# Performance work log

Hardware: AMD Instinct MI355X
Metric: run time of the kernel (lower is better)

Reference implementation:

```python
import jax, jax.numpy as jnp
import numpy as np

B, T, F2, F1 = 64, 300, 2944, 1472
RED, H, K, LN = 256, 32, 15, 7          # reduced_size, hidden_size, att_frams, layer_num
CA_RED = 320
N_CROP = T - 2 * (K - 1)                # 272 frames after the two k=15 convs
PYR = [2 ** j for j in range(1, LN)]    # [2,4,8,16,32,64]


def _pool_matrix(N, sizes):
    """Stacked AdaptiveAvgPool1d matrices: rows average torch-style bins."""
    mats = []
    for m in sizes:
        P = np.zeros((m, N), np.float32)
        for i in range(m):
            s = (i * N) // m
            e = -((-(i + 1) * N) // m)  # ceil((i+1)*N/m)
            P[i, s:e] = 1.0 / (e - s)
        mats.append(P)
    return jnp.asarray(np.concatenate(mats, 0))  # [sum(sizes), N]


def setup_inputs() -> dict:
    key = jax.random.key(0)
    ks = jax.random.split(key, 24)
    g = lambda k, sh, s=0.05: (jax.random.normal(k, sh) * s).astype(jnp.float32)
    inp = {
        "input": jax.random.normal(ks[0], (B, T, F2), jnp.float32),
        "input_length": jnp.full((B,), T, jnp.int64),
        "mean_var": g(ks[1], (F1,), 1.0),
        "std_var": jax.random.uniform(ks[2], (F1,), jnp.float32, 0.5, 1.5),
        "mean_mean": g(ks[3], (F1,), 1.0),
        "std_mean": jax.random.uniform(ks[4], (F1,), jnp.float32, 0.5, 1.5),
        # ChannelAttention params
        "ca_fc1_w": g(ks[5], (CA_RED, F2)), "ca_fc1_b": g(ks[6], (CA_RED,)),
        "ca_fc2_w": g(ks[7], (F2, CA_RED)), "ca_fc2_b": g(ks[8], (F2,)),
        # ANN (n_ANNlayers=1 -> only fc0 used)
        "ann_w": g(ks[9], (RED, F1)), "ann_b": g(ks[10], (RED,)),
        # GRU (torch gate order r,z,n)
        "gru_w_ih": g(ks[11], (3 * H, RED)), "gru_w_hh": g(ks[12], (3 * H, H)),
        "gru_b_ih": g(ks[13], (3 * H,)), "gru_b_hh": g(ks[14], (3 * H,)),
        # frame-quality head
        "q_w": g(ks[15], (1, H)), "q_b": g(ks[16], (1,)),
        # temporal attention convs
        "att_w1": g(ks[17], (1, H, K)), "att_b1": g(ks[18], (1,)),
        "att_w2": g(ks[19], (1, 1, K)), "att_b2": g(ks[20], (1,)),
        "qreg2_w": g(ks[21], (1, 2 ** LN - 1)), "qreg2_b": g(ks[22], (1,)),
    }
    return inp


def _gru(x, w_ih, w_hh, b_ih, b_hh):
    xg = jnp.einsum("btf,gf->btg", x, w_ih) + b_ih  # [B,T,3H]

    def step(h, xt):
        hg = h @ w_hh.T + b_hh
        xr, xz, xn = jnp.split(xt, 3, -1)
        hr, hz, hn = jnp.split(hg, 3, -1)
        r = jax.nn.sigmoid(xr + hr)
        z = jax.nn.sigmoid(xz + hz)
        n = jnp.tanh(xn + r * hn)
        h = (1.0 - z) * n + z * h
        return h, h

    h0 = jnp.zeros((x.shape[0], H), x.dtype)
    _, hs = jax.lax.scan(step, h0, jnp.swapaxes(xg, 0, 1))
    return jnp.swapaxes(hs, 0, 1)  # [B,T,H]


def reference(input, input_length, mean_var, std_var, mean_mean, std_mean,
              ca_fc1_w, ca_fc1_b, ca_fc2_w, ca_fc2_b, ann_w, ann_b,
              gru_w_ih, gru_w_hh, gru_b_ih, gru_b_hh, q_w, q_b,
              att_w1, att_b1, att_w2, att_b2, qreg2_w, qreg2_b):
    # --- ChannelAttention: normalize var/mean halves, sigmoid gate, fuse to 1472-d
    x_var = (input[..., :F1] - mean_var) / std_var
    x_mean = (input[..., F1:] - mean_mean) / std_mean
    xn = jnp.concatenate([x_var, x_mean], -1)                      # [B,T,2944]
    w = jax.nn.sigmoid(jnp.maximum(xn @ ca_fc1_w.T + ca_fc1_b, 0.0) @ ca_fc2_w.T + ca_fc2_b)
    feat = w[..., :F1] * x_var + w[..., F1:] * x_mean              # [B,T,1472]

    # --- ANN (single layer) + GRU
    feat = feat @ ann_w.T + ann_b                                  # [B,T,256]
    outs = _gru(feat, gru_w_ih, gru_w_hh, gru_b_ih, gru_b_hh)      # [B,T,32]

    # --- temporal attention: Conv1d(H,1,15) -> ReLU -> Conv1d(1,1,15) -> tanh
    xc = jnp.swapaxes(outs, 1, 2)                                  # [B,H,T]
    dn = ("NCH", "OIH", "NCH")
    a = jax.lax.conv_general_dilated(xc, att_w1, (1,), "VALID", dimension_numbers=dn) + att_b1[None, :, None]
    a = jnp.maximum(a, 0.0)
    a = jax.lax.conv_general_dilated(a, att_w2, (1,), "VALID", dimension_numbers=dn) + att_b2[None, :, None]
    att = jnp.tanh(a[:, 0, :])                                     # [B,N_CROP]

    q_fet = att[..., None] * outs[:, K - 1: T - (K - 1), :]        # [B,N_CROP,H]

    # --- pyramid pooling: row0 = plain mean, rest = attention-weighted means
    P = _pool_matrix(N_CROP, PYR)                                  # [126, N_CROP]
    row0 = q_fet.mean(1, keepdims=True)                            # [B,1,H]
    num = jnp.einsum("mn,bnh->bmh", P, q_fet)                      # [B,126,H]
    den = jnp.einsum("mn,bn->bm", P, att)[..., None]               # [B,126,1]
    q_pool = jnp.concatenate([row0, num / den], 1)                 # [B,127,H]

    q_each = (q_pool @ q_w.T + q_b)[..., 0]                        # [B,127]
    score = q_each @ qreg2_w.T + qreg2_b                           # [B,1]
    return score
```

## Files before the change

### kernel.cpp

```cpp
#include <hip/hip_runtime.h>


typedef unsigned short u16t;
typedef unsigned int   u32t;
typedef float  f32x4 __attribute__((ext_vector_type(4)));
typedef u32t   u32x4 __attribute__((ext_vector_type(4)));
typedef __bf16 bf16x8 __attribute__((ext_vector_type(8)));

__device__ __forceinline__ f32x4 mfma_b(u32x4 a, u32x4 b, f32x4 c){
  return __builtin_amdgcn_mfma_f32_16x16x32_bf16(
      __builtin_bit_cast(bf16x8, a), __builtin_bit_cast(bf16x8, b), c, 0, 0, 0);
}

#define GLDS16(SRC, DST)                                                    \
  __builtin_amdgcn_global_load_lds(                                         \
      (const __attribute__((address_space(1))) void*)(SRC),                 \
      (__attribute__((address_space(3))) void*)(DST), 16, 0, 0)

__device__ __forceinline__ void split3(float x, u16t& h, u16t& m, u16t& l){
  u32t u = __float_as_uint(x);
  h = (u16t)(u >> 16);
  float d1 = x - __uint_as_float(u & 0xFFFF0000u);
  u32t u1 = __float_as_uint(d1);
  m = (u16t)(u1 >> 16);
  float d2 = d1 - __uint_as_float(u1 & 0xFFFF0000u);
  l = (u16t)(__float_as_uint(d2) >> 16);
}

__device__ __forceinline__ u32t resid(u32t u){
  float d = __uint_as_float(u) - __uint_as_float(u & 0xFFFF0000u);
  return __float_as_uint(d);
}

__device__ __forceinline__ void split8_3(u32x4 a, u32x4 b,
                                         u32x4& H, u32x4& M, u32x4& L){
  u32t r1[8], r2[8];
#pragma unroll
  for (int j = 0; j < 4; j++){ r1[j] = resid(a[j]); r1[4 + j] = resid(b[j]); }
#pragma unroll
  for (int j = 0; j < 8; j++){ r2[j] = resid(r1[j]); }
  H[0] = __builtin_amdgcn_perm(a[1], a[0], 0x07060302u);
  H[1] = __builtin_amdgcn_perm(a[3], a[2], 0x07060302u);
  H[2] = __builtin_amdgcn_perm(b[1], b[0], 0x07060302u);
  H[3] = __builtin_amdgcn_perm(b[3], b[2], 0x07060302u);
  M[0] = __builtin_amdgcn_perm(r1[1], r1[0], 0x07060302u);
  M[1] = __builtin_amdgcn_perm(r1[3], r1[2], 0x07060302u);
  M[2] = __builtin_amdgcn_perm(r1[5], r1[4], 0x07060302u);
  M[3] = __builtin_amdgcn_perm(r1[7], r1[6], 0x07060302u);
  L[0] = __builtin_amdgcn_perm(r2[1], r2[0], 0x07060302u);
  L[1] = __builtin_amdgcn_perm(r2[3], r2[2], 0x07060302u);
  L[2] = __builtin_amdgcn_perm(r2[5], r2[4], 0x07060302u);
  L[3] = __builtin_amdgcn_perm(r2[7], r2[6], 0x07060302u);
}

__device__ __forceinline__ void mfma6(const u32x4& AH, const u32x4& AM, const u32x4& AL,
                                      const u32x4& BH, const u32x4& BM, const u32x4& BL,
                                      f32x4& acc){
  acc = mfma_b(AL, BH, acc);
  acc = mfma_b(AM, BM, acc);
  acc = mfma_b(AH, BL, acc);
  acc = mfma_b(AM, BH, acc);
  acc = mfma_b(AH, BM, acc);
  acc = mfma_b(AH, BH, acc);
}

__global__ __launch_bounds__(256) void prep_params_kernel(
    const float* __restrict__ mv, const float* __restrict__ sv,
    const float* __restrict__ mm, const float* __restrict__ sm,
    double* __restrict__ mu, double* __restrict__ rinv){
  int f = blockIdx.x * 256 + threadIdx.x;
  if (f < 2944){
    if (f < 1472){ mu[f] = (double)mv[f]; rinv[f] = 1.0 / (double)sv[f]; }
    else         { mu[f] = (double)mm[f - 1472]; rinv[f] = 1.0 / (double)sm[f - 1472]; }
  }
}

__global__ __launch_bounds__(256) void split3_w1_kernel(
    const float* __restrict__ w, const double* __restrict__ rinv,
    u16t* __restrict__ wh, u16t* __restrict__ wm, u16t* __restrict__ wl){
  int id = blockIdx.x * 256 + threadIdx.x;
  if (id < 320 * 2944){
    float v = (float)((double)w[id] * rinv[id % 2944]);
    split3(v, wh[id], wm[id], wl[id]);
  }
}

__global__ __launch_bounds__(256) void split3_plain_kernel(
    const float* __restrict__ w, u16t* __restrict__ wh, u16t* __restrict__ wm,
    u16t* __restrict__ wl, int n){
  int id = blockIdx.x * 256 + threadIdx.x;
  if (id < n) split3(w[id], wh[id], wm[id], wl[id]);
}

__global__ __launch_bounds__(64) void b1p_kernel(
    const float* __restrict__ w1, const float* __restrict__ b1,
    const double* __restrict__ mu, const double* __restrict__ rinv,
    float* __restrict__ b1p){
  int n = blockIdx.x, lane = threadIdx.x;
  double s = 0.0;
  for (int k = lane; k < 2944; k += 64)
    s += (double)w1[n * 2944 + k] * rinv[k] * mu[k];
#pragma unroll
  for (int o = 32; o > 0; o >>= 1) s += __shfl_xor(s, o);
  if (lane == 0) b1p[n] = (float)((double)b1[n] - s);
}

__global__ __launch_bounds__(256) void make_wc_kernel(
    const float* __restrict__ wih, const float* __restrict__ annw,
    const float* __restrict__ annb, const float* __restrict__ bih,
    u16t* __restrict__ wch, u16t* __restrict__ wcm, u16t* __restrict__ wcl,
    float* __restrict__ bc){
  int id = blockIdx.x * 256 + threadIdx.x;
  if (id < 96 * 1472){
    int g = id / 1472, k = id - g * 1472;
    double s = 0.0;
    for (int r = 0; r < 256; r++)
      s += (double)wih[g * 256 + r] * (double)annw[r * 1472 + k];
    split3((float)s, wch[id], wcm[id], wcl[id]);
  } else if (id < 96 * 1472 + 96){
    int g = id - 96 * 1472;
    double s = (double)bih[g];
    for (int r = 0; r < 256; r++)
      s += (double)wih[g * 256 + r] * (double)annb[r];
    bc[g] = (float)s;
  }
}

__global__ __launch_bounds__(256) void gemm1_kernel(
    const float* __restrict__ x,
    const u16t* __restrict__ w1h, const u16t* __restrict__ w1m,
    const u16t* __restrict__ w1l, const float* __restrict__ b1p,
    u16t* __restrict__ h1h, u16t* __restrict__ h1m, u16t* __restrict__ h1l){
  __shared__ float lA[64 * 32];
  __shared__ u16t lBh[160 * 32], lBm[160 * 32], lBl[160 * 32];
  const int tid = threadIdx.x, wave = tid >> 6, lane = tid & 63;
  const int wm = wave >> 1, wn = wave & 1;
  const int bid = blockIdx.x;
  const int xcd = bid & 7, j = bid >> 3;
  const int mg = xcd + ((j >> 1) << 3);
  if (mg >= 300) return;
  const int m0 = mg * 64, n0 = (j & 1) * 160;
  const int ar = lane >> 3, as = lane & 7;
  const int br = lane >> 2, bs = lane & 3;
  f32x4 acc[2][5] = {};
  for (int k0 = 0; k0 < 2944; k0 += 32){
    __syncthreads();
#pragma unroll
    for (int i = wave; i < 8; i += 4){
      int row = i * 8 + ar;
      GLDS16(x + (size_t)(m0 + row) * 2944 + k0 + ((as ^ (row & 7)) << 2), lA + (i << 8));
    }
    for (int i = wave; i < 10; i += 4){
      int row = i * 16 + br;
      size_t src = (size_t)(n0 + row) * 2944 + k0 + ((bs ^ ((row >> 1) & 3)) << 3);
      GLDS16(w1h + src, lBh + (i << 9));
      GLDS16(w1m + src, lBm + (i << 9));
      GLDS16(w1l + src, lBl + (i << 9));
    }
    __syncthreads();
    const int g = lane >> 4, r15 = lane & 15;
    u32x4 AH[2], AM[2], AL[2];
#pragma unroll
    for (int fm = 0; fm < 2; fm++){
      int row = wm * 32 + fm * 16 + r15;
      const char* base = (const char*)lA + (row << 7);
      u32x4 a0 = *(const u32x4*)(base + ((((g << 1) + 0) ^ (row & 7)) << 4));
      u32x4 a1 = *(const u32x4*)(base + ((((g << 1) + 1) ^ (row & 7)) << 4));
      split8_3(a0, a1, AH[fm], AM[fm], AL[fm]);
    }
#pragma unroll
    for (int fn = 0; fn < 5; fn++){
      int row = wn * 80 + fn * 16 + r15;
      int off = (row << 6) + ((g ^ ((row >> 1) & 3)) << 4);
      u32x4 BH = *(const u32x4*)((const char*)lBh + off);
      u32x4 BM = *(const u32x4*)((const char*)lBm + off);
      u32x4 BL = *(const u32x4*)((const char*)lBl + off);
#pragma unroll
      for (int fm = 0; fm < 2; fm++)
        mfma6(AH[fm], AM[fm], AL[fm], BH, BM, BL, acc[fm][fn]);
    }
  }
#pragma unroll
  for (int fn = 0; fn < 5; fn++){
    int col = n0 + wn * 80 + fn * 16 + (lane & 15);
    float bias = b1p[col];
#pragma unroll
    for (int fm = 0; fm < 2; fm++){
      int mb = m0 + wm * 32 + fm * 16 + ((lane >> 4) << 2);
#pragma unroll
      for (int r = 0; r < 4; r++){
        float v = fmaxf(acc[fm][fn][r] + bias, 0.f);
        size_t o = (size_t)(mb + r) * 320 + col;
        split3(v, h1h[o], h1m[o], h1l[o]);
      }
    }
  }
}

__global__ __launch_bounds__(256) void gemm2_kernel(
    const u16t* __restrict__ h1h, const u16t* __restrict__ h1m,
    const u16t* __restrict__ h1l,
    const u16t* __restrict__ w2h, const u16t* __restrict__ w2m,
    const u16t* __restrict__ w2l, const float* __restrict__ b2,
    const float* __restrict__ x, const double* __restrict__ mu,
    const double* __restrict__ rinv,
    u16t* __restrict__ feath, u16t* __restrict__ featm, u16t* __restrict__ featl){
  __shared__ u16t lAh[96 * 32], lAm[96 * 32], lAl[96 * 32];
  __shared__ u16t lBh[128 * 32], lBm[128 * 32], lBl[128 * 32];
  const int tid = threadIdx.x, wave = tid >> 6, lane = tid & 63;
  const int wm = wave >> 1, wn = wave & 1;
  const int bid = blockIdx.x;
  const int xcd = bid & 7, j = bid >> 3;
  const int q = j / 23, f0i = j - q * 23;
  const int mg = xcd + (q << 3);
  if (mg >= 200) return;
  const int m0 = mg * 96, f0 = f0i * 64;
  const int br = lane >> 2, bs = lane & 3;
  f32x4 acc[3][4] = {};
  for (int k0 = 0; k0 < 320; k0 += 32){
    __syncthreads();
    for (int i = wave; i < 6; i += 4){
      int row = i * 16 + br;
      int cs = (bs ^ ((row >> 1) & 3)) << 3;
      size_t sa = (size_t)(m0 + row) * 320 + k0 + cs;
      GLDS16(h1h + sa, lAh + (i << 9));
      GLDS16(h1m + sa, lAm + (i << 9));
      GLDS16(h1l + sa, lAl + (i << 9));
    }
    for (int i = wave; i < 8; i += 4){
      int row = i * 16 + br;
      int cs = (bs ^ ((row >> 1) & 3)) << 3;
      int w2row = (((row >> 4) & 1) * 1472) + f0 + ((row >> 5) << 4) + (row & 15);
      size_t sb = (size_t)w2row * 320 + k0 + cs;
      GLDS16(w2h + sb, lBh + (i << 9));
      GLDS16(w2m + sb, lBm + (i << 9));
      GLDS16(w2l + sb, lBl + (i << 9));
    }
    __syncthreads();
    const int g = lane >> 4, r15 = lane & 15;
    u32x4 AH[3], AM[3], AL[3];
#pragma unroll
    for (int fm = 0; fm < 3; fm++){
      int row = wm * 48 + fm * 16 + r15;
      int off = (row << 6) + ((g ^ ((row >> 1) & 3)) << 4);
      AH[fm] = *(const u32x4*)((const char*)lAh + off);
      AM[fm] = *(const u32x4*)((const char*)lAm + off);
      AL[fm] = *(const u32x4*)((const char*)lAl + off);
    }
#pragma unroll
    for (int fn = 0; fn < 4; fn++){
      int row = wn * 64 + fn * 16 + r15;
      int off = (row << 6) + ((g ^ ((row >> 1) & 3)) << 4);
      u32x4 BH = *(const u32x4*)((const char*)lBh + off);
      u32x4 BM = *(const u32x4*)((const char*)lBm + off);
      u32x4 BL = *(const u32x4*)((const char*)lBl + off);
#pragma unroll
      for (int fm = 0; fm < 3; fm++)
        mfma6(AH[fm], AM[fm], AL[fm], BH, BM, BL, acc[fm][fn]);
    }
  }
#pragma unroll
  for (int cg = 0; cg < 2; cg++){
    int f = f0 + wn * 32 + cg * 16 + (lane & 15);
    float blo = b2[f], bhi = b2[1472 + f];
    double muv = mu[f], riv = rinv[f];
    double mum = mu[1472 + f], rim = rinv[1472 + f];
#pragma unroll
    for (int fm = 0; fm < 3; fm++){
      int mb = m0 + wm * 48 + fm * 16 + ((lane >> 4) << 2);
#pragma unroll
      for (int r = 0; r < 4; r++){
        int m = mb + r;
        float zl = acc[fm][2 * cg][r] + blo;
        float zh = acc[fm][2 * cg + 1][r] + bhi;
        float wl = 1.f / (1.f + expf(-zl));
        float wh = 1.f / (1.f + expf(-zh));
        float xv = (float)(((double)x[(size_t)m * 2944 + f] - muv) * riv);
        float xm = (float)(((double)x[(size_t)m * 2944 + 1472 + f] - mum) * rim);
        float fv = wl * xv + wh * xm;
        size_t o = (size_t)m * 1472 + f;
        split3(fv, feath[o], featm[o], featl[o]);
      }
    }
  }
}

__global__ __launch_bounds__(256) void gemm3_kernel(
    const u16t* __restrict__ feath, const u16t* __restrict__ featm,
    const u16t* __restrict__ featl,
    const u16t* __restrict__ wch, const u16t* __restrict__ wcm,
    const u16t* __restrict__ wcl, const float* __restrict__ bc,
    float* __restrict__ xg){
  __shared__ u16t lAh[64 * 32], lAm[64 * 32], lAl[64 * 32];
  __shared__ u16t lBh[96 * 32], lBm[96 * 32], lBl[96 * 32];
  const int tid = threadIdx.x, wave = tid >> 6, lane = tid & 63;
  const int wm = wave >> 1, wn = wave & 1;
  const int m0 = blockIdx.x * 64;
  const int br = lane >> 2, bs = lane & 3;
  f32x4 acc[2][3] = {};
  for (int k0 = 0; k0 < 1472; k0 += 32){
    __syncthreads();
#pragma unroll
    for (int i = wave; i < 4; i += 4){
      int row = i * 16 + br;
      int cs = (bs ^ ((row >> 1) & 3)) << 3;
      size_t sa = (size_t)(m0 + row) * 1472 + k0 + cs;
      GLDS16(feath + sa, lAh + (i << 9));
      GLDS16(featm + sa, lAm + (i << 9));
      GLDS16(featl + sa, lAl + (i << 9));
    }
    for (int i = wave; i < 6; i += 4){
      int row = i * 16 + br;
      int cs = (bs ^ ((row >> 1) & 3)) << 3;
      size_t sb = (size_t)row * 1472 + k0 + cs;
      GLDS16(wch + sb, lBh + (i << 9));
      GLDS16(wcm + sb, lBm + (i << 9));
      GLDS16(wcl + sb, lBl + (i << 9));
    }
    __syncthreads();
    const int g = lane >> 4, r15 = lane & 15;
    u32x4 AH[2], AM[2], AL[2];
#pragma unroll
    for (int fm = 0; fm < 2; fm++){
      int row = wm * 32 + fm * 16 + r15;
      int off = (row << 6) + ((g ^ ((row >> 1) & 3)) << 4);
      AH[fm] = *(const u32x4*)((const char*)lAh + off);
      AM[fm] = *(const u32x4*)((const char*)lAm + off);
      AL[fm] = *(const u32x4*)((const char*)lAl + off);
    }
#pragma unroll
    for (int fn = 0; fn < 3; fn++){
      int row = wn * 48 + fn * 16 + r15;
      int off = (row << 6) + ((g ^ ((row >> 1) & 3)) << 4);
      u32x4 BH = *(const u32x4*)((const char*)lBh + off);
      u32x4 BM = *(const u32x4*)((const char*)lBm + off);
      u32x4 BL = *(const u32x4*)((const char*)lBl + off);
#pragma unroll
      for (int fm = 0; fm < 2; fm++)
        mfma6(AH[fm], AM[fm], AL[fm], BH, BM, BL, acc[fm][fn]);
    }
  }
#pragma unroll
  for (int fn = 0; fn < 3; fn++){
    int col = wn * 48 + fn * 16 + (lane & 15);
    float bias = bc[col];
#pragma unroll
    for (int fm = 0; fm < 2; fm++){
      int mb = m0 + wm * 32 + fm * 16 + ((lane >> 4) << 2);
#pragma unroll
      for (int r = 0; r < 4; r++)
        xg[(size_t)(mb + r) * 96 + col] = acc[fm][fn][r] + bias;
    }
  }
}

__global__ __launch_bounds__(128) void gru_kernel(
    const float* __restrict__ xg, const float* __restrict__ whh,
    const float* __restrict__ bhh, float* __restrict__ outs){
  const int b = blockIdx.x, tid = threadIdx.x;
  __shared__ float hs[32];
  __shared__ double hg[96];
  double wr[32];
  double bias = 0.0;
  if (tid < 96){
#pragma unroll
    for (int j = 0; j < 32; j++) wr[j] = (double)whh[tid * 32 + j];
    bias = (double)bhh[tid];
  }
  if (tid < 32) hs[tid] = 0.f;
  __syncthreads();
  const float* xb = xg + (size_t)b * 300 * 96;
  float* ob = outs + (size_t)b * 300 * 32;
  for (int t = 0; t < 300; t++){
    if (tid < 96){
      double s0 = 0.0, s1 = 0.0;
#pragma unroll
      for (int j = 0; j < 16; j++){
        s0 += wr[j] * (double)hs[j];
        s1 += wr[16 + j] * (double)hs[16 + j];
      }
      hg[tid] = bias + s0 + s1;
    }
    __syncthreads();
    if (tid < 32){
      float xr  = xb[t * 96 + tid];
      float xz  = xb[t * 96 + 32 + tid];
      float xnv = xb[t * 96 + 64 + tid];
      float r = 1.f / (1.f + expf(-(float)((double)xr + hg[tid])));
      float z = 1.f / (1.f + expf(-(float)((double)xz + hg[32 + tid])));
      float n = tanhf((float)((double)xnv + (double)r * hg[64 + tid]));
      float h = (1.f - z) * n + z * hs[tid];
      hs[tid] = h;
      ob[t * 32 + tid] = h;
    }
    __syncthreads();
  }
}

__global__ __launch_bounds__(64) void attn_final_kernel(
    const float* __restrict__ outs, const float* __restrict__ w1,
    const float* __restrict__ b1, const float* __restrict__ w2,
    const float* __restrict__ b2, const float* __restrict__ qw,
    const float* __restrict__ qb, const float* __restrict__ rw,
    const float* __restrict__ rb, float* __restrict__ out){
  const int b = blockIdx.x, lane = threadIdx.x;
  __shared__ float a1[286];
  __shared__ double attv[272];
  __shared__ double sd[272];
  __shared__ float w1s[480];
  __shared__ float qws[32];
  const float* ob = outs + (size_t)b * 300 * 32;
  for (int i = lane; i < 480; i += 64) w1s[i] = w1[i];
  if (lane < 32) qws[lane] = qw[lane];
  __syncthreads();
  const double bb1 = (double)b1[0];
  for (int t = lane; t < 286; t += 64){
    double s = bb1;
    for (int k = 0; k < 15; k++){
      const float* row = ob + (t + k) * 32;
#pragma unroll
      for (int c = 0; c < 32; c++) s += (double)row[c] * (double)w1s[c * 15 + k];
    }
    a1[t] = fmaxf((float)s, 0.f);
  }
  __syncthreads();
  const double bb2 = (double)b2[0];
  for (int t = lane; t < 272; t += 64){
    double s = bb2;
#pragma unroll
    for (int k = 0; k < 15; k++) s += (double)a1[t + k] * (double)w2[k];
    double a = tanh(s);
    attv[t] = a;
    const float* row = ob + (t + 14) * 32;
    double d = 0.0;
#pragma unroll
    for (int c = 0; c < 32; c++) d += (double)row[c] * (double)qws[c];
    sd[t] = a * d;
  }
  __syncthreads();
  const double qb0 = (double)qb[0];
  double part = 0.0;
  double msum = 0.0;
  for (int t = lane; t < 272; t += 64) msum += sd[t];
  part += (double)rw[0] * (msum / 272.0);
  if (lane == 0) part += (double)rw[0] * qb0 + (double)rb[0];
  for (int j = lane; j < 126; j += 64){
    int mcur = 2, i = j;
    while (i >= mcur){ i -= mcur; mcur <<= 1; }
    int s = (i * 272) / mcur;
    int e = ((i + 1) * 272 + mcur - 1) / mcur;
    double S = 0.0, A = 0.0;
    for (int n = s; n < e; n++){ S += sd[n]; A += attv[n]; }
    part += (double)rw[1 + j] * (S / A + qb0);
  }
#pragma unroll
  for (int o = 32; o > 0; o >>= 1) part += __shfl_xor(part, o);
  if (lane == 0) out[b] = (float)part;
}

extern "C" void kernel_launch(void* const* d_in, const int* in_sizes, int n_in,
                              void* d_out, int out_size, void* d_ws, size_t ws_size,
                              hipStream_t stream){
  const float* input     = (const float*)d_in[0];
  const float* mean_var  = (const float*)d_in[2];
  const float* std_var   = (const float*)d_in[3];
  const float* mean_mean = (const float*)d_in[4];
  const float* std_mean  = (const float*)d_in[5];
  const float* ca1w = (const float*)d_in[6];
  const float* ca1b = (const float*)d_in[7];
  const float* ca2w = (const float*)d_in[8];
  const float* ca2b = (const float*)d_in[9];
  const float* annw = (const float*)d_in[10];
  const float* annb = (const float*)d_in[11];
  const float* wih  = (const float*)d_in[12];
  const float* whh  = (const float*)d_in[13];
  const float* bih  = (const float*)d_in[14];
  const float* bhh  = (const float*)d_in[15];
  const float* qw   = (const float*)d_in[16];
  const float* qb   = (const float*)d_in[17];
  const float* aw1  = (const float*)d_in[18];
  const float* ab1  = (const float*)d_in[19];
  const float* aw2  = (const float*)d_in[20];
  const float* ab2  = (const float*)d_in[21];
  const float* rw   = (const float*)d_in[22];
  const float* rb   = (const float*)d_in[23];
  float* out = (float*)d_out;

  char* ws = (char*)d_ws;
  size_t off = 0;
  auto alloc = [&](size_t bytes){
    size_t o = off; off += (bytes + 255) & ~(size_t)255; return o;
  };
  const size_t H1 = (size_t)19200 * 320, FT = (size_t)19200 * 1472;
  u16t* h1h = (u16t*)(ws + alloc(H1 * 2));
  u16t* h1m = (u16t*)(ws + alloc(H1 * 2));
  u16t* h1l = (u16t*)(ws + alloc(H1 * 2));
  u16t* feath = (u16t*)(ws + alloc(FT * 2));
  u16t* featm = (u16t*)(ws + alloc(FT * 2));
  u16t* featl = (u16t*)(ws + alloc(FT * 2));
  float* xg    = (float*)(ws + alloc((size_t)19200 * 96 * 4));
  float* outsb = (float*)(ws + alloc((size_t)19200 * 32 * 4));
  u16t* w1h = (u16t*)(ws + alloc((size_t)320 * 2944 * 2));
  u16t* w1m = (u16t*)(ws + alloc((size_t)320 * 2944 * 2));
  u16t* w1l = (u16t*)(ws + alloc((size_t)320 * 2944 * 2));
  u16t* w2h = (u16t*)(ws + alloc((size_t)2944 * 320 * 2));
  u16t* w2m = (u16t*)(ws + alloc((size_t)2944 * 320 * 2));
  u16t* w2l = (u16t*)(ws + alloc((size_t)2944 * 320 * 2));
  u16t* wch = (u16t*)(ws + alloc((size_t)96 * 1472 * 2));
  u16t* wcm = (u16t*)(ws + alloc((size_t)96 * 1472 * 2));
  u16t* wcl = (u16t*)(ws + alloc((size_t)96 * 1472 * 2));
  double* mu   = (double*)(ws + alloc(2944 * 8));
  double* rinv = (double*)(ws + alloc(2944 * 8));
  float* b1p   = (float*)(ws + alloc(320 * 4));
  float* bc    = (float*)(ws + alloc(96 * 4));
  (void)ws_size; (void)in_sizes; (void)n_in; (void)out_size;

  prep_params_kernel<<<12, 256, 0, stream>>>(mean_var, std_var, mean_mean, std_mean, mu, rinv);
  split3_w1_kernel<<<3680, 256, 0, stream>>>(ca1w, rinv, w1h, w1m, w1l);
  split3_plain_kernel<<<3680, 256, 0, stream>>>(ca2w, w2h, w2m, w2l, 2944 * 320);
  b1p_kernel<<<320, 64, 0, stream>>>(ca1w, ca1b, mu, rinv, b1p);
  make_wc_kernel<<<553, 256, 0, stream>>>(wih, annw, annb, bih, wch, wcm, wcl, bc);
  gemm1_kernel<<<608, 256, 0, stream>>>(input, w1h, w1m, w1l, b1p, h1h, h1m, h1l);
  gemm2_kernel<<<4600, 256, 0, stream>>>(h1h, h1m, h1l, w2h, w2m, w2l, ca2b,
                                         input, mu, rinv, feath, featm, featl);
  gemm3_kernel<<<300, 256, 0, stream>>>(feath, featm, featl, wch, wcm, wcl, bc, xg);
  gru_kernel<<<64, 128, 0, stream>>>(xg, whh, bhh, outsb);
  attn_final_kernel<<<64, 64, 0, stream>>>(outsb, aw1, ab1, aw2, ab2, qw, qb, rw, rb, out);
}
```

Baseline: 926.6 us.

## Fuse channel-attention gating GEMM with GRU input projection via LDS-resident features

Merges gemm2 and gemm3 into one kernel. Each block owns 32 rows and loops over all 23 feature tiles, writing the gated feature tile (split into three bf16 parts) into swizzled LDS. It then immediately multiplies that tile by the combined GRU input weights, which are re-laid out by make_wc_kernel so they can be read directly from global memory. This removes the large three-part feature round-trip through HBM and one kernel launch. The cost is a much smaller M tile, which lowers MFMA reuse per B load, and re-streaming all w2 tiles once per 32-row block, which raises L2 traffic.

```diff
diff --git a/kernel.cpp b/kernel.cpp
--- a/kernel.cpp
+++ b/kernel.cpp
@@ -108,7 +108,7 @@
 __global__ __launch_bounds__(256) void make_wc_kernel(
     const float* __restrict__ wih, const float* __restrict__ annw,
     const float* __restrict__ annb, const float* __restrict__ bih,
-    u16t* __restrict__ wch, u16t* __restrict__ wcm, u16t* __restrict__ wcl,
+    u16t* __restrict__ wcfh, u16t* __restrict__ wcfm, u16t* __restrict__ wcfl,
     float* __restrict__ bc){
   int id = blockIdx.x * 256 + threadIdx.x;
   if (id < 96 * 1472){
@@ -116,7 +116,9 @@
     double s = 0.0;
     for (int r = 0; r < 256; r++)
       s += (double)wih[g * 256 + r] * (double)annw[r * 1472 + k];
-    split3((float)s, wch[id], wcm[id], wcl[id]);
+    size_t o = ((size_t)(k >> 3) * 96 + g) * 8 + (k & 7);
+    u16t hh, mm2, ll; split3((float)s, hh, mm2, ll);
+    wcfh[o] = hh; wcfm[o] = mm2; wcfl[o] = ll;
   } else if (id < 96 * 1472 + 96){
     int g = id - 96 * 1472;
     double s = (double)bih[g];
@@ -197,160 +199,117 @@
   }
 }
 
-__global__ __launch_bounds__(256) void gemm2_kernel(
+__global__ __launch_bounds__(256) void gemm23_kernel(
     const u16t* __restrict__ h1h, const u16t* __restrict__ h1m,
     const u16t* __restrict__ h1l,
     const u16t* __restrict__ w2h, const u16t* __restrict__ w2m,
     const u16t* __restrict__ w2l, const float* __restrict__ b2,
     const float* __restrict__ x, const double* __restrict__ mu,
     const double* __restrict__ rinv,
-    u16t* __restrict__ feath, u16t* __restrict__ featm, u16t* __restrict__ featl){
-  __shared__ u16t lAh[96 * 32], lAm[96 * 32], lAl[96 * 32];
+    const u16t* __restrict__ wcfh, const u16t* __restrict__ wcfm,
+    const u16t* __restrict__ wcfl, const float* __restrict__ bc,
+    float* __restrict__ xg){
+  __shared__ u16t lAh[32 * 32], lAm[32 * 32], lAl[32 * 32];
   __shared__ u16t lBh[128 * 32], lBm[128 * 32], lBl[128 * 32];
+  __shared__ u16t fSh[32 * 64], fSm[32 * 64], fSl[32 * 64];
   const int tid = threadIdx.x, wave = tid >> 6, lane = tid & 63;
   const int wm = wave >> 1, wn = wave & 1;
   const int bid = blockIdx.x;
-  const int xcd = bid & 7, j = bid >> 3;
-  const int q = j / 23, f0i = j - q * 23;
-  const int mg = xcd + (q << 3);
-  if (mg >= 200) return;
-  const int m0 = mg * 96, f0 = f0i * 64;
+  const int mg = (bid & 7) * 75 + (bid >> 3);
+  const int m0 = mg * 32;
   const int br = lane >> 2, bs = lane & 3;
-  f32x4 acc[3][4] = {};
-  for (int k0 = 0; k0 < 320; k0 += 32){
-    __syncthreads();
-    for (int i = wave; i < 6; i += 4){
-      int row = i * 16 + br;
-      int cs = (bs ^ ((row >> 1) & 3)) << 3;
-      size_t sa = (size_t)(m0 + row) * 320 + k0 + cs;
-      GLDS16(h1h + sa, lAh + (i << 9));
-      GLDS16(h1m + sa, lAm + (i << 9));
-      GLDS16(h1l + sa, lAl + (i << 9));
-    }
-    for (int i = wave; i < 8; i += 4){
-      int row = i * 16 + br;
-      int cs = (bs ^ ((row >> 1) & 3)) << 3;
-      int w2row = (((row >> 4) & 1) * 1472) + f0 + ((row >> 5) << 4) + (row & 15);
-      size_t sb = (size_t)w2row * 320 + k0 + cs;
-      GLDS16(w2h + sb, lBh + (i << 9));
-      GLDS16(w2m + sb, lBm + (i << 9));
-      GLDS16(w2l + sb, lBl + (i << 9));
-    }
-    __syncthreads();
-    const int g = lane >> 4, r15 = lane & 15;
-    u32x4 AH[3], AM[3], AL[3];
-#pragma unroll
-    for (int fm = 0; fm < 3; fm++){
-      int row = wm * 48 + fm * 16 + r15;
-      int off = (row << 6) + ((g ^ ((row >> 1) & 3)) << 4);
-      AH[fm] = *(const u32x4*)((const char*)lAh + off);
-      AM[fm] = *(const u32x4*)((const char*)lAm + off);
-      AL[fm] = *(const u32x4*)((const char*)lAl + off);
-    }
-#pragma unroll
-    for (int fn = 0; fn < 4; fn++){
-      int row = wn * 64 + fn * 16 + r15;
-      int off = (row << 6) + ((g ^ ((row >> 1) & 3)) << 4);
-      u32x4 BH = *(const u32x4*)((const char*)lBh + off);
-      u32x4 BM = *(const u32x4*)((const char*)lBm + off);
-      u32x4 BL = *(const u32x4*)((const char*)lBl + off);
-#pragma unroll
-      for (int fm = 0; fm < 3; fm++)
-        mfma6(AH[fm], AM[fm], AL[fm], BH, BM, BL, acc[fm][fn]);
-    }
-  }
-#pragma unroll
-  for (int cg = 0; cg < 2; cg++){
-    int f = f0 + wn * 32 + cg * 16 + (lane & 15);
-    float blo = b2[f], bhi = b2[1472 + f];
-    double muv = mu[f], riv = rinv[f];
-    double mum = mu[1472 + f], rim = rinv[1472 + f];
-#pragma unroll
-    for (int fm = 0; fm < 3; fm++){
-      int mb = m0 + wm * 48 + fm * 16 + ((lane >> 4) << 2);
+  const int g = lane >> 4, r15 = lane & 15;
+  f32x4 acc2[3] = {};
+  for (int f0i = 0; f0i < 23; ++f0i){
+    const int f0 = f0i * 64;
+    f32x4 acc[4] = {};
+    for (int k0 = 0; k0 < 320; k0 += 32){
+      __syncthreads();
+      for (int i = wave; i < 2; i += 4){
+        int row = i * 16 + br;
+        int cs = (bs ^ ((row >> 1) & 3)) << 3;
+        size_t sa = (size_t)(m0 + row) * 320 + k0 + cs;
+        GLDS16(h1h + sa, lAh + (i << 9));
+        GLDS16(h1m + sa, lAm + (i << 9));
+        GLDS16(h1l + sa, lAl + (i << 9));
+      }
+      for (int i = wave; i < 8; i += 4){
+        int row = i * 16 + br;
+        int cs = (bs ^ ((row >> 1) & 3)) << 3;
+        int w2row = (((row >> 4) & 1) * 1472) + f0 + ((row >> 5) << 4) + (row & 15);
+        size_t sb = (size_t)w2row * 320 + k0 + cs;
+        GLDS16(w2h + sb, lBh + (i << 9));
+        GLDS16(w2m + sb, lBm + (i << 9));
+        GLDS16(w2l + sb, lBl + (i << 9));
+      }
+      __syncthreads();
+      int arow = wm * 16 + r15;
+      int aoff = (arow << 6) + ((g ^ ((arow >> 1) & 3)) << 4);
+      u32x4 AH = *(const u32x4*)((const char*)lAh + aoff);
+      u32x4 AM = *(const u32x4*)((const char*)lAm + aoff);
+      u32x4 AL = *(const u32x4*)((const char*)lAl + aoff);
+#pragma unroll
+      for (int fn = 0; fn < 4; fn++){
+        int row = wn * 64 + fn * 16 + r15;
+        int off = (row << 6) + ((g ^ ((row >> 1) & 3)) << 4);
+        u32x4 BH = *(const u32x4*)((const char*)lBh + off);
+        u32x4 BM = *(const u32x4*)((const char*)lBm + off);
+        u32x4 BL = *(const u32x4*)((const char*)lBl + off);
+        mfma6(AH, AM, AL, BH, BM, BL, acc[fn]);
+      }
+    }
+#pragma unroll
+    for (int cg = 0; cg < 2; cg++){
+      int f = f0 + wn * 32 + cg * 16 + r15;
+      float blo = b2[f], bhi = b2[1472 + f];
+      double muv = mu[f], riv = rinv[f];
+      double mum = mu[1472 + f], rim = rinv[1472 + f];
+      int c = wn * 32 + cg * 16 + r15;
+      int mbl = wm * 16 + (g << 2);
 #pragma unroll
       for (int r = 0; r < 4; r++){
-        int m = mb + r;
-        float zl = acc[fm][2 * cg][r] + blo;
-        float zh = acc[fm][2 * cg + 1][r] + bhi;
+        int m = m0 + mbl + r;
+        float zl = acc[2 * cg][r] + blo;
+        float zh = acc[2 * cg + 1][r] + bhi;
         float wl = 1.f / (1.f + expf(-zl));
         float wh = 1.f / (1.f + expf(-zh));
         float xv = (float)(((double)x[(size_t)m * 2944 + f] - muv) * riv);
         float xm = (float)(((double)x[(size_t)m * 2944 + 1472 + f] - mum) * rim);
         float fv = wl * xv + wh * xm;
-        size_t o = (size_t)m * 1472 + f;
-        split3(fv, feath[o], featm[o], featl[o]);
-      }
-    }
-  }
-}
-
-__global__ __launch_bounds__(256) void gemm3_kernel(
-    const u16t* __restrict__ feath, const u16t* __restrict__ featm,
-    const u16t* __restrict__ featl,
-    const u16t* __restrict__ wch, const u16t* __restrict__ wcm,
-    const u16t* __restrict__ wcl, const float* __restrict__ bc,
-    float* __restrict__ xg){
-  __shared__ u16t lAh[64 * 32], lAm[64 * 32], lAl[64 * 32];
-  __shared__ u16t lBh[96 * 32], lBm[96 * 32], lBl[96 * 32];
-  const int tid = threadIdx.x, wave = tid >> 6, lane = tid & 63;
-  const int wm = wave >> 1, wn = wave & 1;
-  const int m0 = blockIdx.x * 64;
-  const int br = lane >> 2, bs = lane & 3;
-  f32x4 acc[2][3] = {};
-  for (int k0 = 0; k0 < 1472; k0 += 32){
+        int lm = mbl + r;
+        int idx = (lm << 6) + (((c >> 3) ^ (lm & 7)) << 3) + (c & 7);
+        u16t hh, mm2, ll; split3(fv, hh, mm2, ll);
+        fSh[idx] = hh; fSm[idx] = mm2; fSl[idx] = ll;
+      }
+    }
     __syncthreads();
 #pragma unroll
-    for (int i = wave; i < 4; i += 4){
-      int row = i * 16 + br;
-      int cs = (bs ^ ((row >> 1) & 3)) << 3;
-      size_t sa = (size_t)(m0 + row) * 1472 + k0 + cs;
-      GLDS16(feath + sa, lAh + (i << 9));
-      GLDS16(featm + sa, lAm + (i << 9));
-      GLDS16(featl + sa, lAl + (i << 9));
-    }
-    for (int i = wave; i < 6; i += 4){
-      int row = i * 16 + br;
-      int cs = (bs ^ ((row >> 1) & 3)) << 3;
-      size_t sb = (size_t)row * 1472 + k0 + cs;
-      GLDS16(wch + sb, lBh + (i << 9));
-      GLDS16(wcm + sb, lBm + (i << 9));
-      GLDS16(wcl + sb, lBl + (i << 9));
-    }
-    __syncthreads();
-    const int g = lane >> 4, r15 = lane & 15;
-    u32x4 AH[2], AM[2], AL[2];
-#pragma unroll
-    for (int fm = 0; fm < 2; fm++){
-      int row = wm * 32 + fm * 16 + r15;
-      int off = (row << 6) + ((g ^ ((row >> 1) & 3)) << 4);
-      AH[fm] = *(const u32x4*)((const char*)lAh + off);
-      AM[fm] = *(const u32x4*)((const char*)lAm + off);
-      AL[fm] = *(const u32x4*)((const char*)lAl + off);
-    }
-#pragma unroll
-    for (int fn = 0; fn < 3; fn++){
-      int row = wn * 48 + fn * 16 + r15;
-      int off = (row << 6) + ((g ^ ((row >> 1) & 3)) << 4);
-      u32x4 BH = *(const u32x4*)((const char*)lBh + off);
-      u32x4 BM = *(const u32x4*)((const char*)lBm + off);
-      u32x4 BL = *(const u32x4*)((const char*)lBl + off);
-#pragma unroll
-      for (int fm = 0; fm < 2; fm++)
-        mfma6(AH[fm], AM[fm], AL[fm], BH, BM, BL, acc[fm][fn]);
+    for (int ks = 0; ks < 2; ks++){
+      int arow = wm * 16 + r15;
+      int slot = (ks * 4 + g) ^ (arow & 7);
+      int aoff = (arow << 7) + (slot << 4);
+      u32x4 AH = *(const u32x4*)((const char*)fSh + aoff);
+      u32x4 AM = *(const u32x4*)((const char*)fSm + aoff);
+      u32x4 AL = *(const u32x4*)((const char*)fSl + aoff);
+#pragma unroll
+      for (int fn = 0; fn < 3; fn++){
+        int grow = wn * 48 + fn * 16 + r15;
+        size_t woff = ((size_t)(f0i * 8 + ks * 4 + g) * 96 + grow) * 8;
+        u32x4 BH = *(const u32x4*)(wcfh + woff);
+        u32x4 BM = *(const u32x4*)(wcfm + woff);
+        u32x4 BL = *(const u32x4*)(wcfl + woff);
+        mfma6(AH, AM, AL, BH, BM, BL, acc2[fn]);
+      }
     }
   }
 #pragma unroll
   for (int fn = 0; fn < 3; fn++){
-    int col = wn * 48 + fn * 16 + (lane & 15);
+    int col = wn * 48 + fn * 16 + r15;
     float bias = bc[col];
-#pragma unroll
-    for (int fm = 0; fm < 2; fm++){
-      int mb = m0 + wm * 32 + fm * 16 + ((lane >> 4) << 2);
-#pragma unroll
-      for (int r = 0; r < 4; r++)
-        xg[(size_t)(mb + r) * 96 + col] = acc[fm][fn][r] + bias;
-    }
+    int mb = m0 + wm * 16 + (g << 2);
+#pragma unroll
+    for (int r = 0; r < 4; r++)
+      xg[(size_t)(mb + r) * 96 + col] = acc2[fn][r] + bias;
   }
 }
 
@@ -491,13 +450,10 @@
   auto alloc = [&](size_t bytes){
     size_t o = off; off += (bytes + 255) & ~(size_t)255; return o;
   };
-  const size_t H1 = (size_t)19200 * 320, FT = (size_t)19200 * 1472;
+  const size_t H1 = (size_t)19200 * 320;
   u16t* h1h = (u16t*)(ws + alloc(H1 * 2));
   u16t* h1m = (u16t*)(ws + alloc(H1 * 2));
   u16t* h1l = (u16t*)(ws + alloc(H1 * 2));
-  u16t* feath = (u16t*)(ws + alloc(FT * 2));
-  u16t* featm = (u16t*)(ws + alloc(FT * 2));
-  u16t* featl = (u16t*)(ws + alloc(FT * 2));
   float* xg    = (float*)(ws + alloc((size_t)19200 * 96 * 4));
   float* outsb = (float*)(ws + alloc((size_t)19200 * 32 * 4));
   u16t* w1h = (u16t*)(ws + alloc((size_t)320 * 2944 * 2));
@@ -506,9 +462,9 @@
   u16t* w2h = (u16t*)(ws + alloc((size_t)2944 * 320 * 2));
   u16t* w2m = (u16t*)(ws + alloc((size_t)2944 * 320 * 2));
   u16t* w2l = (u16t*)(ws + alloc((size_t)2944 * 320 * 2));
-  u16t* wch = (u16t*)(ws + alloc((size_t)96 * 1472 * 2));
-  u16t* wcm = (u16t*)(ws + alloc((size_t)96 * 1472 * 2));
-  u16t* wcl = (u16t*)(ws + alloc((size_t)96 * 1472 * 2));
+  u16t* wcfh = (u16t*)(ws + alloc((size_t)96 * 1472 * 2));
+  u16t* wcfm = (u16t*)(ws + alloc((size_t)96 * 1472 * 2));
+  u16t* wcfl = (u16t*)(ws + alloc((size_t)96 * 1472 * 2));
   double* mu   = (double*)(ws + alloc(2944 * 8));
   double* rinv = (double*)(ws + alloc(2944 * 8));
   float* b1p   = (float*)(ws + alloc(320 * 4));
@@ -519,11 +475,10 @@
   split3_w1_kernel<<<3680, 256, 0, stream>>>(ca1w, rinv, w1h, w1m, w1l);
   split3_plain_kernel<<<3680, 256, 0, stream>>>(ca2w, w2h, w2m, w2l, 2944 * 320);
   b1p_kernel<<<320, 64, 0, stream>>>(ca1w, ca1b, mu, rinv, b1p);
-  make_wc_kernel<<<553, 256, 0, stream>>>(wih, annw, annb, bih, wch, wcm, wcl, bc);
+  make_wc_kernel<<<553, 256, 0, stream>>>(wih, annw, annb, bih, wcfh, wcfm, wcfl, bc);
   gemm1_kernel<<<608, 256, 0, stream>>>(input, w1h, w1m, w1l, b1p, h1h, h1m, h1l);
-  gemm2_kernel<<<4600, 256, 0, stream>>>(h1h, h1m, h1l, w2h, w2m, w2l, ca2b,
-                                         input, mu, rinv, feath, featm, featl);
-  gemm3_kernel<<<300, 256, 0, stream>>>(feath, featm, featl, wch, wcm, wcl, bc, xg);
+  gemm23_kernel<<<600, 256, 0, stream>>>(h1h, h1m, h1l, w2h, w2m, w2l, ca2b,
+                                         input, mu, rinv, wcfh, wcfm, wcfl, bc, xg);
   gru_kernel<<<64, 128, 0, stream>>>(xg, whh, bhh, outsb);
   attn_final_kernel<<<64, 64, 0, stream>>>(outsb, aw1, ab1, aw2, ab2, qw, qb, rw, rb, out);
 }
```

Measured after the change: 1.034 ms. 11.6% more time.

## Retile GEMM kernels to 512-thread blocks with XCD-aware block mapping

Applied to the files above, without the earlier changes.

Gemm1 moves to 512-thread blocks, with each wave owning a 16-row slice and blocks mapped so each XCD works on a contiguous M range and a fixed N half. Gemm2 doubles its M tile to 192 with 512 threads and uses an XCD-chunked work index. Gemm3 halves its M tile to 32 rows to launch more blocks. Several B/A loads switch from direct global-to-LDS loads to register-staged copies. The aim is better occupancy, L2 locality per XCD and more parallelism, at the cost of less reuse per wave and possibly lower load efficiency from the register staging.

```diff
diff --git a/kernel.cpp b/kernel.cpp
--- a/kernel.cpp
+++ b/kernel.cpp
@@ -126,7 +126,7 @@
   }
 }
 
-__global__ __launch_bounds__(256) void gemm1_kernel(
+__global__ __launch_bounds__(512) void gemm1_kernel(
     const float* __restrict__ x,
     const u16t* __restrict__ w1h, const u16t* __restrict__ w1m,
     const u16t* __restrict__ w1l, const float* __restrict__ b1p,
@@ -137,36 +137,38 @@
   const int wm = wave >> 1, wn = wave & 1;
   const int bid = blockIdx.x;
   const int xcd = bid & 7, j = bid >> 3;
-  const int mg = xcd + ((j >> 1) << 3);
-  if (mg >= 300) return;
-  const int m0 = mg * 64, n0 = (j & 1) * 160;
+  const int n0 = (xcd & 4) ? 160 : 0;
+  const int m0 = ((xcd & 3) * 75 + j) * 64;
   const int ar = lane >> 3, as = lane & 7;
   const int br = lane >> 2, bs = lane & 3;
-  f32x4 acc[2][5] = {};
+  const int g = lane >> 4, r15 = lane & 15;
+  f32x4 acc[5] = {};
   for (int k0 = 0; k0 < 2944; k0 += 32){
     __syncthreads();
-#pragma unroll
-    for (int i = wave; i < 8; i += 4){
+    {
+      int i = wave;
       int row = i * 8 + ar;
       GLDS16(x + (size_t)(m0 + row) * 2944 + k0 + ((as ^ (row & 7)) << 2), lA + (i << 8));
     }
-    for (int i = wave; i < 10; i += 4){
+    for (int i = wave; i < 10; i += 8){
       int row = i * 16 + br;
       size_t src = (size_t)(n0 + row) * 2944 + k0 + ((bs ^ ((row >> 1) & 3)) << 3);
-      GLDS16(w1h + src, lBh + (i << 9));
-      GLDS16(w1m + src, lBm + (i << 9));
-      GLDS16(w1l + src, lBl + (i << 9));
-    }
-    __syncthreads();
-    const int g = lane >> 4, r15 = lane & 15;
-    u32x4 AH[2], AM[2], AL[2];
-#pragma unroll
-    for (int fm = 0; fm < 2; fm++){
-      int row = wm * 32 + fm * 16 + r15;
+      uint4 vh = *(const uint4*)(w1h + src);
+      uint4 vm = *(const uint4*)(w1m + src);
+      uint4 vl = *(const uint4*)(w1l + src);
+      int d = (i << 9) + (lane << 3);
+      *(uint4*)(lBh + d) = vh;
+      *(uint4*)(lBm + d) = vm;
+      *(uint4*)(lBl + d) = vl;
+    }
+    __syncthreads();
+    u32x4 AH, AM, AL;
+    {
+      int row = wm * 16 + r15;
       const char* base = (const char*)lA + (row << 7);
       u32x4 a0 = *(const u32x4*)(base + ((((g << 1) + 0) ^ (row & 7)) << 4));
       u32x4 a1 = *(const u32x4*)(base + ((((g << 1) + 1) ^ (row & 7)) << 4));
-      split8_3(a0, a1, AH[fm], AM[fm], AL[fm]);
+      split8_3(a0, a1, AH, AM, AL);
     }
 #pragma unroll
     for (int fn = 0; fn < 5; fn++){
@@ -175,29 +177,24 @@
       u32x4 BH = *(const u32x4*)((const char*)lBh + off);
       u32x4 BM = *(const u32x4*)((const char*)lBm + off);
       u32x4 BL = *(const u32x4*)((const char*)lBl + off);
-#pragma unroll
-      for (int fm = 0; fm < 2; fm++)
-        mfma6(AH[fm], AM[fm], AL[fm], BH, BM, BL, acc[fm][fn]);
+      mfma6(AH, AM, AL, BH, BM, BL, acc[fn]);
     }
   }
 #pragma unroll
   for (int fn = 0; fn < 5; fn++){
-    int col = n0 + wn * 80 + fn * 16 + (lane & 15);
+    int col = n0 + wn * 80 + fn * 16 + r15;
     float bias = b1p[col];
-#pragma unroll
-    for (int fm = 0; fm < 2; fm++){
-      int mb = m0 + wm * 32 + fm * 16 + ((lane >> 4) << 2);
-#pragma unroll
-      for (int r = 0; r < 4; r++){
-        float v = fmaxf(acc[fm][fn][r] + bias, 0.f);
-        size_t o = (size_t)(mb + r) * 320 + col;
-        split3(v, h1h[o], h1m[o], h1l[o]);
-      }
-    }
-  }
-}
-
-__global__ __launch_bounds__(256) void gemm2_kernel(
+    int mb = m0 + wm * 16 + ((lane >> 4) << 2);
+#pragma unroll
+    for (int r = 0; r < 4; r++){
+      float v = fmaxf(acc[fn][r] + bias, 0.f);
+      size_t o = (size_t)(mb + r) * 320 + col;
+      split3(v, h1h[o], h1m[o], h1l[o]);
+    }
+  }
+}
+
+__global__ __launch_bounds__(512) void gemm2_kernel(
     const u16t* __restrict__ h1h, const u16t* __restrict__ h1m,
     const u16t* __restrict__ h1l,
     const u16t* __restrict__ w2h, const u16t* __restrict__ w2m,
@@ -205,29 +202,34 @@
     const float* __restrict__ x, const double* __restrict__ mu,
     const double* __restrict__ rinv,
     u16t* __restrict__ feath, u16t* __restrict__ featm, u16t* __restrict__ featl){
-  __shared__ u16t lAh[96 * 32], lAm[96 * 32], lAl[96 * 32];
+  __shared__ u16t lAh[192 * 32], lAm[192 * 32], lAl[192 * 32];
   __shared__ u16t lBh[128 * 32], lBm[128 * 32], lBl[128 * 32];
   const int tid = threadIdx.x, wave = tid >> 6, lane = tid & 63;
   const int wm = wave >> 1, wn = wave & 1;
   const int bid = blockIdx.x;
-  const int xcd = bid & 7, j = bid >> 3;
-  const int q = j / 23, f0i = j - q * 23;
-  const int mg = xcd + (q << 3);
-  if (mg >= 200) return;
-  const int m0 = mg * 96, f0 = f0i * 64;
+  const int work = (bid & 7) * 288 + (bid >> 3);
+  if (work >= 2300) return;
+  const int mg = work / 23, f0i = work - mg * 23;
+  const int m0 = mg * 192, f0 = f0i * 64;
   const int br = lane >> 2, bs = lane & 3;
+  const int g = lane >> 4, r15 = lane & 15;
   f32x4 acc[3][4] = {};
   for (int k0 = 0; k0 < 320; k0 += 32){
     __syncthreads();
-    for (int i = wave; i < 6; i += 4){
+    for (int i = wave; i < 12; i += 8){
       int row = i * 16 + br;
       int cs = (bs ^ ((row >> 1) & 3)) << 3;
       size_t sa = (size_t)(m0 + row) * 320 + k0 + cs;
-      GLDS16(h1h + sa, lAh + (i << 9));
-      GLDS16(h1m + sa, lAm + (i << 9));
-      GLDS16(h1l + sa, lAl + (i << 9));
-    }
-    for (int i = wave; i < 8; i += 4){
+      uint4 vh = *(const uint4*)(h1h + sa);
+      uint4 vm = *(const uint4*)(h1m + sa);
+      uint4 vl = *(const uint4*)(h1l + sa);
+      int d = (i << 9) + (lane << 3);
+      *(uint4*)(lAh + d) = vh;
+      *(uint4*)(lAm + d) = vm;
+      *(uint4*)(lAl + d) = vl;
+    }
+    {
+      int i = wave;
       int row = i * 16 + br;
       int cs = (bs ^ ((row >> 1) & 3)) << 3;
       int w2row = (((row >> 4) & 1) * 1472) + f0 + ((row >> 5) << 4) + (row & 15);
@@ -237,7 +239,6 @@
       GLDS16(w2l + sb, lBl + (i << 9));
     }
     __syncthreads();
-    const int g = lane >> 4, r15 = lane & 15;
     u32x4 AH[3], AM[3], AL[3];
 #pragma unroll
     for (int fm = 0; fm < 3; fm++){
@@ -261,7 +262,7 @@
   }
 #pragma unroll
   for (int cg = 0; cg < 2; cg++){
-    int f = f0 + wn * 32 + cg * 16 + (lane & 15);
+    int f = f0 + wn * 32 + cg * 16 + r15;
     float blo = b2[f], bhi = b2[1472 + f];
     double muv = mu[f], riv = rinv[f];
     double mum = mu[1472 + f], rim = rinv[1472 + f];
@@ -291,17 +292,18 @@
     const u16t* __restrict__ wch, const u16t* __restrict__ wcm,
     const u16t* __restrict__ wcl, const float* __restrict__ bc,
     float* __restrict__ xg){
-  __shared__ u16t lAh[64 * 32], lAm[64 * 32], lAl[64 * 32];
+  __shared__ u16t lAh[32 * 32], lAm[32 * 32], lAl[32 * 32];
   __shared__ u16t lBh[96 * 32], lBm[96 * 32], lBl[96 * 32];
   const int tid = threadIdx.x, wave = tid >> 6, lane = tid & 63;
   const int wm = wave >> 1, wn = wave & 1;
-  const int m0 = blockIdx.x * 64;
+  const int bid = blockIdx.x;
+  const int m0 = ((bid & 7) * 75 + (bid >> 3)) * 32;
   const int br = lane >> 2, bs = lane & 3;
-  f32x4 acc[2][3] = {};
+  const int g = lane >> 4, r15 = lane & 15;
+  f32x4 acc[3] = {};
   for (int k0 = 0; k0 < 1472; k0 += 32){
     __syncthreads();
-#pragma unroll
-    for (int i = wave; i < 4; i += 4){
+    for (int i = wave; i < 2; i += 4){
       int row = i * 16 + br;
       int cs = (bs ^ ((row >> 1) & 3)) << 3;
       size_t sa = (size_t)(m0 + row) * 1472 + k0 + cs;
@@ -313,20 +315,22 @@
       int row = i * 16 + br;
       int cs = (bs ^ ((row >> 1) & 3)) << 3;
       size_t sb = (size_t)row * 1472 + k0 + cs;
-      GLDS16(wch + sb, lBh + (i << 9));
-      GLDS16(wcm + sb, lBm + (i << 9));
-      GLDS16(wcl + sb, lBl + (i << 9));
-    }
-    __syncthreads();
-    const int g = lane >> 4, r15 = lane & 15;
-    u32x4 AH[2], AM[2], AL[2];
-#pragma unroll
-    for (int fm = 0; fm < 2; fm++){
-      int row = wm * 32 + fm * 16 + r15;
+      uint4 vh = *(const uint4*)(wch + sb);
+      uint4 vm = *(const uint4*)(wcm + sb);
+      uint4 vl = *(const uint4*)(wcl + sb);
+      int d = (i << 9) + (lane << 3);
+      *(uint4*)(lBh + d) = vh;
+      *(uint4*)(lBm + d) = vm;
+      *(uint4*)(lBl + d) = vl;
+    }
+    __syncthreads();
+    u32x4 AH, AM, AL;
+    {
+      int row = wm * 16 + r15;
       int off = (row << 6) + ((g ^ ((row >> 1) & 3)) << 4);
-      AH[fm] = *(const u32x4*)((const char*)lAh + off);
-      AM[fm] = *(const u32x4*)((const char*)lAm + off);
-      AL[fm] = *(const u32x4*)((const char*)lAl + off);
+      AH = *(const u32x4*)((const char*)lAh + off);
+      AM = *(const u32x4*)((const char*)lAm + off);
+      AL = *(const u32x4*)((const char*)lAl + off);
     }
 #pragma unroll
     for (int fn = 0; fn < 3; fn++){
@@ -335,22 +339,17 @@
       u32x4 BH = *(const u32x4*)((const char*)lBh + off);
       u32x4 BM = *(const u32x4*)((const char*)lBm + off);
       u32x4 BL = *(const u32x4*)((const char*)lBl + off);
-#pragma unroll
-      for (int fm = 0; fm < 2; fm++)
-        mfma6(AH[fm], AM[fm], AL[fm], BH, BM, BL, acc[fm][fn]);
+      mfma6(AH, AM, AL, BH, BM, BL, acc[fn]);
     }
   }
 #pragma unroll
   for (int fn = 0; fn < 3; fn++){
-    int col = wn * 48 + fn * 16 + (lane & 15);
+    int col = wn * 48 + fn * 16 + r15;
     float bias = bc[col];
-#pragma unroll
-    for (int fm = 0; fm < 2; fm++){
-      int mb = m0 + wm * 32 + fm * 16 + ((lane >> 4) << 2);
-#pragma unroll
-      for (int r = 0; r < 4; r++)
-        xg[(size_t)(mb + r) * 96 + col] = acc[fm][fn][r] + bias;
-    }
+    int mb = m0 + wm * 16 + ((lane >> 4) << 2);
+#pragma unroll
+    for (int r = 0; r < 4; r++)
+      xg[(size_t)(mb + r) * 96 + col] = acc[fn][r] + bias;
   }
 }
 
@@ -520,10 +519,10 @@
   split3_plain_kernel<<<3680, 256, 0, stream>>>(ca2w, w2h, w2m, w2l, 2944 * 320);
   b1p_kernel<<<320, 64, 0, stream>>>(ca1w, ca1b, mu, rinv, b1p);
   make_wc_kernel<<<553, 256, 0, stream>>>(wih, annw, annb, bih, wch, wcm, wcl, bc);
-  gemm1_kernel<<<608, 256, 0, stream>>>(input, w1h, w1m, w1l, b1p, h1h, h1m, h1l);
-  gemm2_kernel<<<4600, 256, 0, stream>>>(h1h, h1m, h1l, w2h, w2m, w2l, ca2b,
+  gemm1_kernel<<<600, 512, 0, stream>>>(input, w1h, w1m, w1l, b1p, h1h, h1m, h1l);
+  gemm2_kernel<<<2304, 512, 0, stream>>>(h1h, h1m, h1l, w2h, w2m, w2l, ca2b,
                                          input, mu, rinv, feath, featm, featl);
-  gemm3_kernel<<<300, 256, 0, stream>>>(feath, featm, featl, wch, wcm, wcl, bc, xg);
+  gemm3_kernel<<<600, 256, 0, stream>>>(feath, featm, featl, wch, wcm, wcl, bc, xg);
   gru_kernel<<<64, 128, 0, stream>>>(xg, whh, bhh, outsb);
   attn_final_kernel<<<64, 64, 0, stream>>>(outsb, aw1, ab1, aw2, ab2, qw, qb, rw, rb, out);
 }
```

After: 946.3 us. 1.02x slower.
